# Optimization experiments

Hardware: AMD Instinct MI355X
Metric: run time of the kernel (lower is better)

## Reference

```python
import jax, jax.numpy as jnp
import numpy as np
import math

T = 1024
HID = 2880
NH = 64      # attention heads
KV = 8       # key/value heads
HD = 64      # head dim
INTER = 2880
QMULT = NH // KV
SM_SCALE = 1.0 / math.sqrt(HD)
ALPHA = 1.702   # swiglu alpha
LIMIT = 7.0     # swiglu clamp limit
EPS = 1e-5
ROPE_BASE = 150000.0
INIT_CTX = 4096
SCALING = 32.0
NTK_ALPHA = 1.0
NTK_BETA = 32.0


def rmsnorm(x, scale):
    t = x * jax.lax.rsqrt(jnp.mean(x * x, axis=-1, keepdims=True) + EPS)
    return t * scale


def rope_cos_sin(num_tokens):
    # YaRN-style NTK interpolation (scaling_factor > 1 branch)
    freq = ROPE_BASE ** (jnp.arange(0, HD, 2, dtype=jnp.float32) / HD)
    concentration = 0.1 * math.log(SCALING) + 1.0
    d_half = HD / 2
    low = d_half * math.log(INIT_CTX / (NTK_BETA * 2 * math.pi)) / math.log(ROPE_BASE)
    high = d_half * math.log(INIT_CTX / (NTK_ALPHA * 2 * math.pi)) / math.log(ROPE_BASE)
    interpolation = 1.0 / (SCALING * freq)
    extrapolation = 1.0 / freq
    ramp = (jnp.arange(d_half, dtype=jnp.float32) - low) / (high - low)
    mask = 1.0 - jnp.clip(ramp, 0.0, 1.0)
    inv_freq = interpolation * (1.0 - mask) + extrapolation * mask
    t = jnp.arange(num_tokens, dtype=jnp.float32)
    freqs = t[:, None] * inv_freq[None, :]           # [T, HD/2]
    return jnp.cos(freqs) * concentration, jnp.sin(freqs) * concentration


def apply_rope(x, cos, sin):
    # x: [T, heads, HD]; cos/sin: [T, HD/2]
    c = cos[:, None, :]
    s = sin[:, None, :]
    x1, x2 = jnp.split(x, 2, axis=-1)
    return jnp.concatenate([x1 * c - x2 * s, x2 * c + x1 * s], axis=-1)


def setup_inputs() -> dict:
    key = jax.random.key(0)
    ks = jax.random.split(key, 10)
    p = lambda k, shape: jax.random.normal(k, shape, jnp.float32) * 0.02
    qkv_dim = HD * (NH + 2 * KV)
    return {
        "x": jax.random.normal(ks[0], (T, HID), jnp.float32),
        "attn_norm_scale": jnp.ones((HID,), jnp.float32),
        "wqkv": p(ks[1], (qkv_dim, HID)),
        "bqkv": p(ks[2], (qkv_dim,)),
        "wout": p(ks[3], (HID, NH * HD)),
        "bout": p(ks[4], (HID,)),
        "mlp_norm_scale": jnp.ones((HID,), jnp.float32),
        "w1": p(ks[5], (2 * INTER, HID)),
        "b1": p(ks[6], (2 * INTER,)),
        "w2": p(ks[7], (HID, INTER)),
        "b2": p(ks[8], (HID,)),
    }


def reference(x, attn_norm_scale, wqkv, bqkv, wout, bout, mlp_norm_scale, w1, b1, w2, b2):
    # ---- attention sub-block ----
    t = rmsnorm(x, attn_norm_scale)
    qkv = t @ wqkv.T + bqkv                                   # [T, 5120]
    q = qkv[:, : NH * HD].reshape(T, NH, HD)
    k = qkv[:, NH * HD : (NH + KV) * HD].reshape(T, KV, HD)
    v = qkv[:, (NH + KV) * HD :].reshape(T, KV, HD)
    cos, sin = rope_cos_sin(T)
    q = apply_rope(q, cos, sin)
    k = apply_rope(k, cos, sin)
    kf = jnp.repeat(k, QMULT, axis=1)                         # GQA expand -> [T, NH, HD]
    vf = jnp.repeat(v, QMULT, axis=1)
    scores = jnp.einsum('thd,shd->hts', q, kf) * SM_SCALE     # [NH, T, T]
    causal = jnp.tril(jnp.ones((T, T), dtype=bool))
    scores = jnp.where(causal[None, :, :], scores, jnp.float32(-1e30))
    attn = jax.nn.softmax(scores, axis=-1)
    o = jnp.einsum('hts,shd->thd', attn, vf).reshape(T, NH * HD)
    h = x + o @ wout.T + bout                                 # residual
    # ---- SwiGLU MLP sub-block ----
    u = rmsnorm(h, mlp_norm_scale) @ w1.T + b1                # [T, 2*INTER] interleaved
    g = jnp.minimum(u[:, ::2], LIMIT)
    lin = jnp.clip(u[:, 1::2], -LIMIT, LIMIT)
    act = g * jax.nn.sigmoid(ALPHA * g) * (lin + 1.0)         # [T, INTER]
    return h + act @ w2.T + b2
```

## Files before the change

### kernel.cpp

```cpp
#include <hip/hip_runtime.h>

typedef unsigned short ushort_t;
typedef unsigned int uint_t;
typedef __bf16 bf16x8 __attribute__((ext_vector_type(8)));
typedef float floatx4 __attribute__((ext_vector_type(4)));

#define T_TOK 1024
#define HID 2880
#define NH 64
#define KV 8
#define HD 64
#define INTER 2880
#define QKV_DIM 5120
#define O_DIM 4096

typedef __attribute__((address_space(1))) const uint_t glb_u32;
typedef __attribute__((address_space(3))) uint_t lds_u32;

__device__ __forceinline__ float b2f(ushort_t u) {
    uint_t i = ((uint_t)u) << 16;
    return __builtin_bit_cast(float, i);
}
__device__ __forceinline__ ushort_t f2b(float f) {
    uint_t i = __builtin_bit_cast(uint_t, f);
    uint_t r = i + 0x7FFFu + ((i >> 16) & 1u);
    return (ushort_t)(r >> 16);
}
__device__ __forceinline__ uint4 ld16(const void* p) { uint4 v; __builtin_memcpy(&v, p, 16); return v; }
__device__ __forceinline__ void st16(void* p, uint4 v) { __builtin_memcpy(p, &v, 16); }
__device__ __forceinline__ float4 ld16f(const void* p) { float4 v; __builtin_memcpy(&v, p, 16); return v; }
__device__ __forceinline__ bf16x8 ldfrag(const void* p) { bf16x8 v; __builtin_memcpy(&v, p, 16); return v; }
__device__ __forceinline__ void cvt8st(void* lds, float4 a, float4 b) {
    __bf16 o[8] = {(__bf16)a.x, (__bf16)a.y, (__bf16)a.z, (__bf16)a.w,
                   (__bf16)b.x, (__bf16)b.y, (__bf16)b.z, (__bf16)b.w};
    __builtin_memcpy(lds, o, 16);
}

__global__ __launch_bounds__(256) void rmsnorm_f2b(
    const float* __restrict__ x, const float* __restrict__ scale,
    ushort_t* __restrict__ out)
{
    const int row = blockIdx.x;
    const int tid = threadIdx.x;
    const float* xr = x + (size_t)row * HID;
    float ss = 0.f;
    for (int i = tid; i < HID / 4; i += 256) {
        float4 v = ld16f(xr + i * 4);
        ss += v.x * v.x + v.y * v.y + v.z * v.z + v.w * v.w;
    }
    #pragma unroll
    for (int m = 32; m >= 1; m >>= 1) ss += __shfl_xor(ss, m, 64);
    __shared__ float red[4];
    if ((tid & 63) == 0) red[tid >> 6] = ss;
    __syncthreads();
    float rstd = rsqrtf((red[0] + red[1] + red[2] + red[3]) / (float)HID + 1e-5f);
    for (int i = tid; i < HID / 8; i += 256) {
        float4 a = ld16f(xr + i * 8);
        float4 b = ld16f(xr + i * 8 + 4);
        float4 sa = ld16f(scale + i * 8);
        float4 sb = ld16f(scale + i * 8 + 4);
        cvt8st(out + (size_t)row * HID + i * 8,
               make_float4(a.x * rstd * sa.x, a.y * rstd * sa.y, a.z * rstd * sa.z, a.w * rstd * sa.w),
               make_float4(b.x * rstd * sb.x, b.y * rstd * sb.y, b.z * rstd * sb.z, b.w * rstd * sb.w));
    }
}

__global__ __launch_bounds__(256) void gemm_bt(
    const ushort_t* __restrict__ A, const float* __restrict__ B,
    const float* __restrict__ bias, const float* residual,
    void* C, int out_f32, float* __restrict__ scratch,
    int M, int N, int K)
{
    __shared__ ushort_t As[2][128 * 64];
    __shared__ ushort_t Bs[2][64 * 64];
    const int tid = threadIdx.x;
    const int lane = tid & 63, wave = tid >> 6;
    const int l15 = lane & 15, quad = lane >> 4;

    const int nbm = M >> 7;
    int flat = (int)blockIdx.x;
    const int cpx = (int)gridDim.x >> 3;
    flat = (flat & 7) * cpx + (flat >> 3);
    const int m0 = (flat % nbm) * 128;
    const int n0 = (flat / nbm) * 64;

    const int wm = (wave >> 1) * 64, wn = (wave & 1) * 32;

    const int z = (int)blockIdx.y;
    const int nk_all = K >> 6;
    const int nk0 = (nk_all + 1) >> 1;
    const int kbeg = (gridDim.y > 1 && z) ? (nk0 << 6) : 0;
    const int nk = (gridDim.y > 1) ? (z ? nk_all - nk0 : nk0) : nk_all;

    const int arow = wave * 32 + (lane >> 3);
    const int aslot = (lane & 7) ^ (lane >> 3);
    const ushort_t* Abase = A + (size_t)(m0 + arow) * K + kbeg + aslot * 8;

    const int brow = tid >> 2;
    const int kb = (tid & 3) * 8;
    const int sa = (tid & 3) ^ (brow & 7);
    const int sb = ((tid & 3) + 4) ^ (brow & 7);
    const float* Bbase = B + (size_t)(n0 + brow) * K + kbeg;

    floatx4 acc[4][2] = {};

    {
        float4 f0 = ld16f(Bbase + kb);
        float4 f1 = ld16f(Bbase + kb + 4);
        float4 f2 = ld16f(Bbase + kb + 32);
        float4 f3 = ld16f(Bbase + kb + 36);
        #pragma unroll
        for (int q = 0; q < 4; q++)
            __builtin_amdgcn_global_load_lds(
                (glb_u32*)(Abase + (size_t)(q * 8) * K),
                (lds_u32*)(&As[0][(wave * 4 + q) * 512]), 16, 0, 0);
        cvt8st(&Bs[0][brow * 64 + sa * 8], f0, f1);
        cvt8st(&Bs[0][brow * 64 + sb * 8], f2, f3);
    }

    int cur = 0;
    for (int kt = 0; kt < nk; ++kt) {
        const int nxt = cur ^ 1;
        const bool pre = (kt + 1 < nk);
        float4 f0, f1, f2, f3;
        if (pre) {
            const int k1 = (kt + 1) << 6;
            f0 = ld16f(Bbase + k1 + kb);
            f1 = ld16f(Bbase + k1 + kb + 4);
            f2 = ld16f(Bbase + k1 + kb + 32);
            f3 = ld16f(Bbase + k1 + kb + 36);
            #pragma unroll
            for (int q = 0; q < 4; q++)
                __builtin_amdgcn_global_load_lds(
                    (glb_u32*)(Abase + (size_t)(q * 8) * K + k1),
                    (lds_u32*)(&As[nxt][(wave * 4 + q) * 512]), 16, 0, 0);
            asm volatile("s_waitcnt vmcnt(8)" ::: "memory");
        } else {
            asm volatile("s_waitcnt vmcnt(0)" ::: "memory");
        }
        asm volatile("s_waitcnt lgkmcnt(0)" ::: "memory");
        __builtin_amdgcn_s_barrier();
        __builtin_amdgcn_sched_barrier(0);

        #pragma unroll
        for (int c = 0; c < 2; c++) {
            bf16x8 af[4], bfr[2];
            #pragma unroll
            for (int i = 0; i < 4; i++) {
                int r = wm + i * 16 + l15;
                af[i] = ldfrag(&As[cur][r * 64 + (((c * 4 + quad) ^ (r & 7)) * 8)]);
            }
            #pragma unroll
            for (int j = 0; j < 2; j++) {
                int r = wn + j * 16 + l15;
                bfr[j] = ldfrag(&Bs[cur][r * 64 + (((c * 4 + quad) ^ (r & 7)) * 8)]);
            }
            #pragma unroll
            for (int i = 0; i < 4; i++)
                #pragma unroll
                for (int j = 0; j < 2; j++)
                    acc[i][j] = __builtin_amdgcn_mfma_f32_16x16x32_bf16(af[i], bfr[j], acc[i][j], 0, 0, 0);
        }
        if (pre) {
            cvt8st(&Bs[nxt][brow * 64 + sa * 8], f0, f1);
            cvt8st(&Bs[nxt][brow * 64 + sb * 8], f2, f3);
        }
        __builtin_amdgcn_s_barrier();
        cur = nxt;
    }

    if (gridDim.y > 1 && z) {
        #pragma unroll
        for (int i = 0; i < 4; i++) {
            int row = m0 + wm + i * 16 + quad * 4;
            #pragma unroll
            for (int j = 0; j < 2; j++) {
                int col = n0 + wn + j * 16 + l15;
                #pragma unroll
                for (int r = 0; r < 4; r++)
                    scratch[(size_t)(row + r) * N + col] = acc[i][j][r];
            }
        }
        return;
    }
    #pragma unroll
    for (int i = 0; i < 4; i++) {
        int row = m0 + wm + i * 16 + quad * 4;
        #pragma unroll
        for (int j = 0; j < 2; j++) {
            int col = n0 + wn + j * 16 + l15;
            float bv = bias[col];
            #pragma unroll
            for (int r = 0; r < 4; r++) {
                float v = acc[i][j][r] + bv;
                if (residual) v += residual[(size_t)(row + r) * N + col];
                if (out_f32) ((float*)C)[(size_t)(row + r) * N + col] = v;
                else ((ushort_t*)C)[(size_t)(row + r) * N + col] = f2b(v);
            }
        }
    }
}

__global__ __launch_bounds__(256) void add_inplace(
    float* __restrict__ dst, const float* __restrict__ src)
{
    int i = (blockIdx.x * 256 + threadIdx.x) * 4;
    float4 a = ld16f(dst + i);
    float4 b = ld16f(src + i);
    a.x += b.x; a.y += b.y; a.z += b.z; a.w += b.w;
    __builtin_memcpy(dst + i, &a, 16);
}

__global__ __launch_bounds__(256) void rope_kernel(ushort_t* __restrict__ qkv)
{
    int idx = blockIdx.x * 256 + threadIdx.x;
    int d = idx & 31;
    int rest = idx >> 5;
    int head = rest % (NH + KV);
    int tok = rest / (NH + KV);

    float fd = (float)d;
    float freq = exp2f(fd * (17.194638f / 32.0f));
    float interpolation = 1.0f / (32.0f * freq);
    float extrapolation = 1.0f / freq;
    float ramp = (fd - 8.092761f) * (1.0f / (17.397992f - 8.092761f));
    ramp = fminf(fmaxf(ramp, 0.0f), 1.0f);
    float mask = 1.0f - ramp;
    float inv_freq = interpolation * (1.0f - mask) + extrapolation * mask;
    float ang = (float)tok * inv_freq;
    float s = sinf(ang) * 1.3465736f;
    float c = cosf(ang) * 1.3465736f;

    size_t base = (head < NH)
        ? (size_t)tok * QKV_DIM + head * HD
        : (size_t)tok * QKV_DIM + NH * HD + (head - NH) * HD;
    float x1 = b2f(qkv[base + d]);
    float x2 = b2f(qkv[base + 32 + d]);
    qkv[base + d]      = f2b(x1 * c - x2 * s);
    qkv[base + 32 + d] = f2b(x2 * c + x1 * s);
}

__global__ __launch_bounds__(256) void attn_kernel(
    const ushort_t* __restrict__ qkv, ushort_t* __restrict__ o)
{
    const int qt = blockIdx.x;
    const int h  = blockIdx.y;
    const int g  = h >> 3;
    const int tid = threadIdx.x;
    const int lane = tid & 63, wave = tid >> 6;
    const int l15 = lane & 15, quad = lane >> 4;

    __shared__ ushort_t Ks[64 * 72];
    __shared__ ushort_t Vt[64 * 72];
    __shared__ ushort_t Ps[4][16 * 72];

    bf16x8 qf[2];
    const int qrow = qt * 64 + wave * 16 + l15;
    #pragma unroll
    for (int c = 0; c < 2; c++)
        qf[c] = ldfrag(&qkv[(size_t)qrow * QKV_DIM + h * HD + quad * 8 + 32 * c]);

    floatx4 ofrag[4] = {};
    float mrow[4], lrow[4];
    #pragma unroll
    for (int r = 0; r < 4; r++) { mrow[r] = -1e30f; lrow[r] = 0.f; }

    for (int kt = 0; kt <= qt; ++kt) {
        {
            int row = tid >> 2;
            int seg = (tid & 3) * 16;
            size_t sb = (size_t)(kt * 64 + row) * QKV_DIM + NH * HD + g * HD;
            st16(&Ks[row * 72 + seg],     ld16(&qkv[sb + seg]));
            st16(&Ks[row * 72 + seg + 8], ld16(&qkv[sb + seg + 8]));
            uint4 v0 = ld16(&qkv[sb + KV * HD + seg]);
            uint4 v1 = ld16(&qkv[sb + KV * HD + seg + 8]);
            uint_t w0[4] = {v0.x, v0.y, v0.z, v0.w};
            uint_t w1[4] = {v1.x, v1.y, v1.z, v1.w};
            #pragma unroll
            for (int e = 0; e < 8; e++) {
                ushort_t s0 = (e & 1) ? (ushort_t)(w0[e >> 1] >> 16) : (ushort_t)(w0[e >> 1] & 0xffffu);
                ushort_t s1 = (e & 1) ? (ushort_t)(w1[e >> 1] >> 16) : (ushort_t)(w1[e >> 1] & 0xffffu);
                Vt[(seg + e) * 72 + row]     = s0;
                Vt[(seg + 8 + e) * 72 + row] = s1;
            }
        }
        __syncthreads();

        floatx4 sf[4];
        #pragma unroll
        for (int j = 0; j < 4; j++) {
            floatx4 z = {};
            #pragma unroll
            for (int c = 0; c < 2; c++) {
                bf16x8 kf = ldfrag(&Ks[(j * 16 + l15) * 72 + quad * 8 + 32 * c]);
                z = __builtin_amdgcn_mfma_f32_16x16x32_bf16(qf[c], kf, z, 0, 0, 0);
            }
            sf[j] = z;
        }
        const int qg = qt * 64 + wave * 16 + quad * 4;
        const int kgb = kt * 64 + l15;
        float rowmax[4];
        #pragma unroll
        for (int r = 0; r < 4; r++) rowmax[r] = -1e30f;
        #pragma unroll
        for (int j = 0; j < 4; j++)
            #pragma unroll
            for (int r = 0; r < 4; r++) {
                float v = sf[j][r] * 0.125f;
                if (kgb + j * 16 > qg + r) v = -1e30f;
                sf[j][r] = v;
                rowmax[r] = fmaxf(rowmax[r], v);
            }
        #pragma unroll
        for (int r = 0; r < 4; r++)
            #pragma unroll
            for (int m = 1; m < 16; m <<= 1)
                rowmax[r] = fmaxf(rowmax[r], __shfl_xor(rowmax[r], m, 64));
        float alpha[4], rowsum[4];
        #pragma unroll
        for (int r = 0; r < 4; r++) {
            float mnew = fmaxf(mrow[r], rowmax[r]);
            alpha[r] = __expf(mrow[r] - mnew);
            mrow[r] = mnew;
            rowsum[r] = 0.f;
        }
        #pragma unroll
        for (int j = 0; j < 4; j++)
            #pragma unroll
            for (int r = 0; r < 4; r++) {
                float p = __expf(sf[j][r] - mrow[r]);
                rowsum[r] += p;
                Ps[wave][(quad * 4 + r) * 72 + j * 16 + l15] = f2b(p);
            }
        #pragma unroll
        for (int r = 0; r < 4; r++) {
            #pragma unroll
            for (int m = 1; m < 16; m <<= 1)
                rowsum[r] += __shfl_xor(rowsum[r], m, 64);
            lrow[r] = lrow[r] * alpha[r] + rowsum[r];
        }
        #pragma unroll
        for (int j = 0; j < 4; j++)
            #pragma unroll
            for (int r = 0; r < 4; r++)
                ofrag[j][r] *= alpha[r];
        __syncthreads();
        #pragma unroll
        for (int c = 0; c < 2; c++) {
            bf16x8 pf = ldfrag(&Ps[wave][l15 * 72 + quad * 8 + 32 * c]);
            #pragma unroll
            for (int j = 0; j < 4; j++) {
                bf16x8 vf = ldfrag(&Vt[(j * 16 + l15) * 72 + quad * 8 + 32 * c]);
                ofrag[j] = __builtin_amdgcn_mfma_f32_16x16x32_bf16(pf, vf, ofrag[j], 0, 0, 0);
            }
        }
        __syncthreads();
    }
    #pragma unroll
    for (int j = 0; j < 4; j++)
        #pragma unroll
        for (int r = 0; r < 4; r++) {
            int row = qt * 64 + wave * 16 + quad * 4 + r;
            int col = h * HD + j * 16 + l15;
            o[(size_t)row * O_DIM + col] = f2b(ofrag[j][r] / lrow[r]);
        }
}

__global__ __launch_bounds__(256) void act_kernel(
    const ushort_t* __restrict__ u, ushort_t* __restrict__ act)
{
    int i = blockIdx.x * 256 + threadIdx.x;
    if (i >= T_TOK * INTER) return;
    int row = i / INTER, c = i % INTER;
    uint_t v; __builtin_memcpy(&v, u + (size_t)row * (2 * INTER) + 2 * c, 4);
    float gt  = b2f((ushort_t)(v & 0xffffu));
    float lin = b2f((ushort_t)(v >> 16));
    gt = fminf(gt, 7.0f);
    lin = fminf(fmaxf(lin, -7.0f), 7.0f);
    float sg = 1.0f / (1.0f + __expf(-1.702f * gt));
    act[i] = f2b(gt * sg * (lin + 1.0f));
}

extern "C" void kernel_launch(void* const* d_in, const int* in_sizes, int n_in,
                              void* d_out, int out_size, void* d_ws, size_t ws_size,
                              hipStream_t stream)
{
    const float* x               = (const float*)d_in[0];
    const float* attn_norm_scale = (const float*)d_in[1];
    const float* wqkv            = (const float*)d_in[2];
    const float* bqkv            = (const float*)d_in[3];
    const float* wout            = (const float*)d_in[4];
    const float* bout            = (const float*)d_in[5];
    const float* mlp_norm_scale  = (const float*)d_in[6];
    const float* w1              = (const float*)d_in[7];
    const float* b1              = (const float*)d_in[8];
    const float* w2              = (const float*)d_in[9];
    const float* b2              = (const float*)d_in[10];
    float* out = (float*)d_out;

    char* ws = (char*)d_ws;
    ushort_t* t   = (ushort_t*)ws;
    ushort_t* qkv = (ushort_t*)(ws + (size_t)T_TOK * HID * 2);
    ushort_t* ob  = (ushort_t*)(ws + (size_t)T_TOK * (HID + QKV_DIM) * 2);
    ushort_t* u   = (ushort_t*)(ws + (size_t)T_TOK * (HID + QKV_DIM + O_DIM) * 2);
    ushort_t* ac  = (ushort_t*)(ws + (size_t)T_TOK * (HID + QKV_DIM + O_DIM + 2 * INTER) * 2);
    float* sc1 = (float*)u;
    float* sc2 = (float*)qkv;

    rmsnorm_f2b<<<T_TOK, 256, 0, stream>>>(x, attn_norm_scale, t);
    gemm_bt<<<dim3((T_TOK / 128) * (QKV_DIM / 64)), 256, 0, stream>>>(
        t, wqkv, bqkv, nullptr, qkv, 0, nullptr, T_TOK, QKV_DIM, HID);
    rope_kernel<<<(T_TOK * (NH + KV) * 32) / 256, 256, 0, stream>>>(qkv);
    attn_kernel<<<dim3(T_TOK / 64, NH), 256, 0, stream>>>(qkv, ob);
    gemm_bt<<<dim3((T_TOK / 128) * (HID / 64), 2), 256, 0, stream>>>(
        ob, wout, bout, x, out, 1, sc1, T_TOK, HID, O_DIM);
    add_inplace<<<(T_TOK * HID) / 1024, 256, 0, stream>>>(out, sc1);
    rmsnorm_f2b<<<T_TOK, 256, 0, stream>>>(out, mlp_norm_scale, t);
    gemm_bt<<<dim3((T_TOK / 128) * ((2 * INTER) / 64)), 256, 0, stream>>>(
        t, w1, b1, nullptr, u, 0, nullptr, T_TOK, 2 * INTER, HID);
    act_kernel<<<(T_TOK * INTER + 255) / 256, 256, 0, stream>>>(u, ac);
    gemm_bt<<<dim3((T_TOK / 128) * (HID / 64), 2), 256, 0, stream>>>(
        ac, w2, b2, out, out, 1, sc2, T_TOK, HID, INTER);
    add_inplace<<<(T_TOK * HID) / 1024, 256, 0, stream>>>(out, sc2);
}
```

Baseline: 547.5 us.

## Stream fp32 weights directly to LDS and convert to bf16 at fragment load

The GEMM now copies the fp32 B tile straight into LDS with global_load_lds instead of loading it through registers, converting to bf16 and storing. Conversion moves to fragment-read time. K-tile shrinks from 64 to 32 to fit the larger fp32 tile, and launch bounds request 5 blocks per CU. This is meant to cut VGPR pressure and register round-trips while raising occupancy. In exchange it doubles the number of loop iterations and barriers, and the single barrier per iteration may expose latency.

```diff
diff --git a/kernel.cpp b/kernel.cpp
--- a/kernel.cpp
+++ b/kernel.cpp
@@ -65,14 +65,14 @@
     }
 }
 
-__global__ __launch_bounds__(256) void gemm_bt(
+__global__ __launch_bounds__(256, 5) void gemm_bt(
     const ushort_t* __restrict__ A, const float* __restrict__ B,
     const float* __restrict__ bias, const float* residual,
     void* C, int out_f32, float* __restrict__ scratch,
     int M, int N, int K)
 {
-    __shared__ ushort_t As[2][128 * 64];
-    __shared__ ushort_t Bs[2][64 * 64];
+    __shared__ ushort_t As[2][128 * 32];
+    __shared__ float    Bs[2][64 * 32];
     const int tid = threadIdx.x;
     const int lane = tid & 63, wave = tid >> 6;
     const int l15 = lane & 15, quad = lane >> 4;
@@ -87,86 +87,77 @@
     const int wm = (wave >> 1) * 64, wn = (wave & 1) * 32;
 
     const int z = (int)blockIdx.y;
-    const int nk_all = K >> 6;
+    const int nk_all = K >> 5;
     const int nk0 = (nk_all + 1) >> 1;
-    const int kbeg = (gridDim.y > 1 && z) ? (nk0 << 6) : 0;
+    const int kbeg = (gridDim.y > 1 && z) ? (nk0 << 5) : 0;
     const int nk = (gridDim.y > 1) ? (z ? nk_all - nk0 : nk0) : nk_all;
 
-    const int arow = wave * 32 + (lane >> 3);
-    const int aslot = (lane & 7) ^ (lane >> 3);
-    const ushort_t* Abase = A + (size_t)(m0 + arow) * K + kbeg + aslot * 8;
-
-    const int brow = tid >> 2;
-    const int kb = (tid & 3) * 8;
-    const int sa = (tid & 3) ^ (brow & 7);
-    const int sb = ((tid & 3) + 4) ^ (brow & 7);
-    const float* Bbase = B + (size_t)(n0 + brow) * K + kbeg;
+    const int arow = wave * 32 + (lane >> 2);
+    const int asl = (lane & 3) ^ ((lane >> 2) & 3) ^ ((lane >> 4) & 3);
+    const ushort_t* Abase = A + (size_t)(m0 + arow) * K + kbeg + asl * 8;
+
+    const int brow = wave * 16 + (lane >> 3);
+    const int bsl = (lane & 7) ^ ((lane >> 3) & 7);
+    const float* Bbase = B + (size_t)(n0 + brow) * K + kbeg + bsl * 4;
+
+    const int ar_sl = (quad ^ (l15 & 3) ^ ((l15 >> 2) & 3)) * 8;
+    const int br_lo = ((2 * quad) ^ (l15 & 7)) * 4;
+    const int br_hi = ((2 * quad + 1) ^ (l15 & 7)) * 4;
 
     floatx4 acc[4][2] = {};
 
-    {
-        float4 f0 = ld16f(Bbase + kb);
-        float4 f1 = ld16f(Bbase + kb + 4);
-        float4 f2 = ld16f(Bbase + kb + 32);
-        float4 f3 = ld16f(Bbase + kb + 36);
-        #pragma unroll
-        for (int q = 0; q < 4; q++)
-            __builtin_amdgcn_global_load_lds(
-                (glb_u32*)(Abase + (size_t)(q * 8) * K),
-                (lds_u32*)(&As[0][(wave * 4 + q) * 512]), 16, 0, 0);
-        cvt8st(&Bs[0][brow * 64 + sa * 8], f0, f1);
-        cvt8st(&Bs[0][brow * 64 + sb * 8], f2, f3);
+    #pragma unroll
+    for (int q = 0; q < 2; q++) {
+        __builtin_amdgcn_global_load_lds(
+            (glb_u32*)(Abase + (size_t)(q * 16) * K),
+            (lds_u32*)(&As[0][(wave * 32 + q * 16) * 32]), 16, 0, 0);
+        __builtin_amdgcn_global_load_lds(
+            (glb_u32*)(Bbase + (size_t)(q * 8) * K),
+            (lds_u32*)(&Bs[0][(wave * 16 + q * 8) * 32]), 16, 0, 0);
     }
 
     int cur = 0;
     for (int kt = 0; kt < nk; ++kt) {
-        const int nxt = cur ^ 1;
-        const bool pre = (kt + 1 < nk);
-        float4 f0, f1, f2, f3;
-        if (pre) {
-            const int k1 = (kt + 1) << 6;
-            f0 = ld16f(Bbase + k1 + kb);
-            f1 = ld16f(Bbase + k1 + kb + 4);
-            f2 = ld16f(Bbase + k1 + kb + 32);
-            f3 = ld16f(Bbase + k1 + kb + 36);
-            #pragma unroll
-            for (int q = 0; q < 4; q++)
-                __builtin_amdgcn_global_load_lds(
-                    (glb_u32*)(Abase + (size_t)(q * 8) * K + k1),
-                    (lds_u32*)(&As[nxt][(wave * 4 + q) * 512]), 16, 0, 0);
-            asm volatile("s_waitcnt vmcnt(8)" ::: "memory");
-        } else {
-            asm volatile("s_waitcnt vmcnt(0)" ::: "memory");
-        }
-        asm volatile("s_waitcnt lgkmcnt(0)" ::: "memory");
+        asm volatile("s_waitcnt vmcnt(0)" ::: "memory");
         __builtin_amdgcn_s_barrier();
         __builtin_amdgcn_sched_barrier(0);
 
-        #pragma unroll
-        for (int c = 0; c < 2; c++) {
-            bf16x8 af[4], bfr[2];
-            #pragma unroll
-            for (int i = 0; i < 4; i++) {
-                int r = wm + i * 16 + l15;
-                af[i] = ldfrag(&As[cur][r * 64 + (((c * 4 + quad) ^ (r & 7)) * 8)]);
-            }
-            #pragma unroll
-            for (int j = 0; j < 2; j++) {
-                int r = wn + j * 16 + l15;
-                bfr[j] = ldfrag(&Bs[cur][r * 64 + (((c * 4 + quad) ^ (r & 7)) * 8)]);
-            }
-            #pragma unroll
-            for (int i = 0; i < 4; i++)
-                #pragma unroll
-                for (int j = 0; j < 2; j++)
-                    acc[i][j] = __builtin_amdgcn_mfma_f32_16x16x32_bf16(af[i], bfr[j], acc[i][j], 0, 0, 0);
-        }
-        if (pre) {
-            cvt8st(&Bs[nxt][brow * 64 + sa * 8], f0, f1);
-            cvt8st(&Bs[nxt][brow * 64 + sb * 8], f2, f3);
-        }
-        __builtin_amdgcn_s_barrier();
-        cur = nxt;
+        if (kt + 1 < nk) {
+            const int k1 = (kt + 1) << 5;
+            const int nxt = cur ^ 1;
+            #pragma unroll
+            for (int q = 0; q < 2; q++) {
+                __builtin_amdgcn_global_load_lds(
+                    (glb_u32*)(Abase + (size_t)(q * 16) * K + k1),
+                    (lds_u32*)(&As[nxt][(wave * 32 + q * 16) * 32]), 16, 0, 0);
+                __builtin_amdgcn_global_load_lds(
+                    (glb_u32*)(Bbase + (size_t)(q * 8) * K + k1),
+                    (lds_u32*)(&Bs[nxt][(wave * 16 + q * 8) * 32]), 16, 0, 0);
+            }
+        }
+
+        bf16x8 af[4], bfr[2];
+        #pragma unroll
+        for (int i = 0; i < 4; i++)
+            af[i] = ldfrag(&As[cur][(wm + i * 16 + l15) * 32 + ar_sl]);
+        #pragma unroll
+        for (int j = 0; j < 2; j++) {
+            const float* bp = &Bs[cur][(wn + j * 16 + l15) * 32];
+            float4 lo = ld16f(bp + br_lo);
+            float4 hi = ld16f(bp + br_hi);
+            bf16x8 b;
+            b[0] = (__bf16)lo.x; b[1] = (__bf16)lo.y;
+            b[2] = (__bf16)lo.z; b[3] = (__bf16)lo.w;
+            b[4] = (__bf16)hi.x; b[5] = (__bf16)hi.y;
+            b[6] = (__bf16)hi.z; b[7] = (__bf16)hi.w;
+            bfr[j] = b;
+        }
+        #pragma unroll
+        for (int i = 0; i < 4; i++)
+            #pragma unroll
+            for (int j = 0; j < 2; j++)
+                acc[i][j] = __builtin_amdgcn_mfma_f32_16x16x32_bf16(af[i], bfr[j], acc[i][j], 0, 0, 0);
+        cur ^= 1;
     }
 
     if (gridDim.y > 1 && z) {
```

Result: slower. 621.9 us (+13.6%).
